# Kernel optimization log

Hardware: AMD Instinct MI355X
Metric: run time of the kernel (lower is better)

## Reference

```python
import jax, jax.numpy as jnp
import numpy as np

B, L, H, W = 16, 16, 64, 64
NUM_CODES = 64


def setup_inputs() -> dict:
    key = jax.random.key(0)
    k1, k2 = jax.random.split(key)
    z = jax.random.normal(k1, (B, L, H, W), dtype=jnp.float32)
    # nn.Embedding(latent_dim, num_codes).weight -> [latent_dim, num_codes]
    codes_w = jax.random.normal(k2, (L, NUM_CODES), dtype=jnp.float32)
    return {"z": z, "codes_w": codes_w}


def reference(z, codes_w):
    # z: [B, L, H, W] -> h: [B, H, W, L]
    h = jnp.transpose(z, (0, 2, 3, 1))
    # broadcast abs-distance to every code: [B, H, W, L, C]
    distances = jnp.abs(h[..., None] - codes_w)
    # Softmin over code axis == softmax of negated distances
    symbol_probs = jax.nn.softmax(-distances, axis=-1)
    # soft quantization: probability-weighted codebook values -> [B, H, W, L]
    soft_symbols = jnp.sum(symbol_probs * codes_w, axis=-1)
    # hard assignment: nearest code per (position, latent channel)
    idxes = jnp.argmin(distances, axis=-1)  # [B, H, W, L] int
    # gather codebook value per latent row (equivalent of take with row offsets)
    hard_symbols = jnp.take_along_axis(
        codes_w[None, None, None], idxes[..., None], axis=4
    )[..., 0]
    return soft_symbols, hard_symbols, idxes
```

## Files before the change

### kernel.cpp

```cpp
#include <hip/hip_runtime.h>


namespace {
constexpr int kL = 16;
constexpr int kC = 64;
constexpr int kHW = 64 * 64;
constexpr int kN = 16 * kHW * kL;
constexpr int kStride = 68;
constexpr float kLog2e = 1.44269504088896340736f;
}

__global__ __launch_bounds__(256) void soft_to_hard_kernel(
    const float* __restrict__ z,
    const float* __restrict__ codes,
    float* __restrict__ out)
{
    __shared__ float wl[kL * kStride];
    __shared__ float pl[kL * kStride];
    __shared__ float ql[kL * kStride];

    const int tid = threadIdx.x;

    {
        const int base = tid << 2;
        const int l = base >> 6;
        const int c = base & 63;
        const float4 wv = *reinterpret_cast<const float4*>(codes + base);
        const int o = l * kStride + c;
        wl[o + 0] = wv.x; wl[o + 1] = wv.y; wl[o + 2] = wv.z; wl[o + 3] = wv.w;
        pl[o + 0] = exp2f(wv.x * kLog2e);
        pl[o + 1] = exp2f(wv.y * kLog2e);
        pl[o + 2] = exp2f(wv.z * kLog2e);
        pl[o + 3] = exp2f(wv.w * kLog2e);
        ql[o + 0] = exp2f(-wv.x * kLog2e);
        ql[o + 1] = exp2f(-wv.y * kLog2e);
        ql[o + 2] = exp2f(-wv.z * kLog2e);
        ql[o + 3] = exp2f(-wv.w * kLog2e);
    }
    __syncthreads();

    const int gid = blockIdx.x * 256 + tid;
    const int l   = gid & (kL - 1);
    const int bhw = gid >> 4;
    const int b   = gid >> 16;
    const int hw  = bhw & (kHW - 1);

    const float zv = z[(b << 16) + (l << 12) + hw];

    const float t    = zv * kLog2e;
    const float E    = exp2f(t);
    const float Einv = exp2f(-t);

    const float* __restrict__ wr = wl + l * kStride;
    const float* __restrict__ pr = pl + l * kStride;
    const float* __restrict__ qr = ql + l * kStride;

    float mind = 3.4e38f;
    int   idx  = 0;
    float sum  = 0.0f;
    float wsum = 0.0f;

#define STEP(wc, pc, qc, cc)                                  \
    {                                                         \
        const float d = __builtin_fabsf(zv - (wc));           \
        idx  = (d < mind) ? (cc) : idx;                       \
        mind = fminf(d, mind);                                \
        const float e = fminf(E * (qc), Einv * (pc));         \
        sum += e;                                             \
        wsum = __builtin_fmaf(e, (wc), wsum);                 \
    }

#pragma unroll
    for (int c0 = 0; c0 < kC; c0 += 4) {
        const float4 wv = *reinterpret_cast<const float4*>(wr + c0);
        const float4 pv = *reinterpret_cast<const float4*>(pr + c0);
        const float4 qv = *reinterpret_cast<const float4*>(qr + c0);
        STEP(wv.x, pv.x, qv.x, c0 + 0);
        STEP(wv.y, pv.y, qv.y, c0 + 1);
        STEP(wv.z, pv.z, qv.z, c0 + 2);
        STEP(wv.w, pv.w, qv.w, c0 + 3);
    }
#undef STEP

    const float soft = wsum / sum;
    const float hard = wr[idx];

    out[gid]          = soft;
    out[kN + gid]     = hard;
    out[2 * kN + gid] = (float)idx;
}

extern "C" void kernel_launch(void* const* d_in, const int* in_sizes, int n_in,
                              void* d_out, int out_size, void* d_ws, size_t ws_size,
                              hipStream_t stream) {
    const float* z     = (const float*)d_in[0];
    const float* codes = (const float*)d_in[1];
    float* out = (float*)d_out;

    const int threads = 256;
    const int blocks  = kN / threads;
    soft_to_hard_kernel<<<blocks, threads, 0, stream>>>(z, codes, out);
}
```

Measured before the change: 72.11 us.

## Replace per-element code scan with sorted codebook, binary search and prefix-sum softmin

Each block sorts every codebook row in shared memory with a rank sort, resolves tie indices, and builds forward and backward prefix sums of exp(±w) and w·exp(±w). Each element then binary-searches its sorted row, computes the softmin sums from the two prefix tables with two exps, and picks the nearest code from the two neighbours. Each thread handles 8 elements across batches, with 512 blocks instead of 4096. This removes the 64-code inner loop per element, at the cost of per-block sort and table setup, and of prefix sums whose rounding differs from direct summation.

```diff
diff --git a/kernel.cpp b/kernel.cpp
--- a/kernel.cpp
+++ b/kernel.cpp
@@ -3,91 +3,150 @@
 
 namespace {
 constexpr int kL = 16;
-constexpr int kC = 64;
-constexpr int kHW = 64 * 64;
-constexpr int kN = 16 * kHW * kL;
-constexpr int kStride = 68;
+constexpr int kHW = 4096;
+constexpr int kN = 1 << 20;
+constexpr int kRow = 66;
+constexpr int kKRow = 65;
+constexpr int kTStride = kL * kRow + 12;
 constexpr float kLog2e = 1.44269504088896340736f;
 }
 
-__global__ __launch_bounds__(256) void soft_to_hard_kernel(
+__global__ __launch_bounds__(256) void soft_to_hard_fused(
     const float* __restrict__ z,
     const float* __restrict__ codes,
     float* __restrict__ out)
 {
-    __shared__ float wl[kL * kStride];
-    __shared__ float pl[kL * kStride];
-    __shared__ float ql[kL * kStride];
+    __shared__ unsigned long long K[kL * kKRow];
+    __shared__ float SW[kL * kRow];
+    __shared__ float RP[kL * kRow];
+    __shared__ float tabs[4 * kTStride];
 
     const int tid = threadIdx.x;
+    const int row = tid >> 4;
+    const int c0  = (tid & 15) << 2;
 
-    {
-        const int base = tid << 2;
-        const int l = base >> 6;
-        const int c = base & 63;
-        const float4 wv = *reinterpret_cast<const float4*>(codes + base);
-        const int o = l * kStride + c;
-        wl[o + 0] = wv.x; wl[o + 1] = wv.y; wl[o + 2] = wv.z; wl[o + 3] = wv.w;
-        pl[o + 0] = exp2f(wv.x * kLog2e);
-        pl[o + 1] = exp2f(wv.y * kLog2e);
-        pl[o + 2] = exp2f(wv.z * kLog2e);
-        pl[o + 3] = exp2f(wv.w * kLog2e);
-        ql[o + 0] = exp2f(-wv.x * kLog2e);
-        ql[o + 1] = exp2f(-wv.y * kLog2e);
-        ql[o + 2] = exp2f(-wv.z * kLog2e);
-        ql[o + 3] = exp2f(-wv.w * kLog2e);
+    const float4 wv = *reinterpret_cast<const float4*>(codes + (row << 6) + c0);
+    float v4[4] = {wv.x, wv.y, wv.z, wv.w};
+    unsigned long long myk[4];
+#pragma unroll
+    for (int k = 0; k < 4; ++k) {
+        unsigned int u = __float_as_uint(v4[k]);
+        u ^= (u & 0x80000000u) ? 0xFFFFFFFFu : 0x80000000u;
+        myk[k] = ((unsigned long long)u << 6) | (unsigned long long)(c0 + k);
+        K[row * kKRow + c0 + k] = myk[k];
+    }
+    if (tid < kL) {
+        SW[tid * kRow + 0]  = -3.0e38f;  RP[tid * kRow + 0]  = 1.0e9f;
+        SW[tid * kRow + 65] =  3.0e38f;  RP[tid * kRow + 65] = 1.0e9f;
     }
     __syncthreads();
 
-    const int gid = blockIdx.x * 256 + tid;
-    const int l   = gid & (kL - 1);
-    const int bhw = gid >> 4;
-    const int b   = gid >> 16;
-    const int hw  = bhw & (kHW - 1);
+    {
+        int r[4] = {0, 0, 0, 0};
+        const unsigned long long* Kr = K + row * kKRow;
+#pragma unroll 16
+        for (int c2 = 0; c2 < 64; ++c2) {
+            const unsigned long long k2 = Kr[c2];
+#pragma unroll
+            for (int k = 0; k < 4; ++k) r[k] += (k2 < myk[k]);
+        }
+#pragma unroll
+        for (int k = 0; k < 4; ++k) {
+            SW[row * kRow + r[k] + 1] = v4[k];
+            RP[row * kRow + r[k] + 1] = (float)(c0 + k);
+        }
+    }
+    __syncthreads();
 
-    const float zv = z[(b << 16) + (l << 12) + hw];
+    for (int pass = 0; pass < 2; ++pass) {
+        float nrep[4];
+#pragma unroll
+        for (int k = 0; k < 4; ++k) {
+            const int o = row * kRow + c0 + k + 1;
+            const float a = SW[o], b = SW[o - 1];
+            nrep[k] = (a == b) ? fminf(RP[o], RP[o - 1]) : RP[o];
+        }
+        __syncthreads();
+#pragma unroll
+        for (int k = 0; k < 4; ++k) RP[row * kRow + c0 + k + 1] = nrep[k];
+        __syncthreads();
+    }
 
-    const float t    = zv * kLog2e;
-    const float E    = exp2f(t);
-    const float Einv = exp2f(-t);
+    if (tid < 64) {
+        const int drow = tid >> 2;
+        const int kind = tid & 3;
+        const bool fwd = kind < 2;
+        const bool wgt = (kind & 1) != 0;
+        float* T = tabs + kind * kTStride + drow * kRow;
+        const float* S = SW + drow * kRow;
+        const float sgn = fwd ? kLog2e : -kLog2e;
+        float acc = 0.0f;
+        T[fwd ? 0 : 64] = 0.0f;
+        T[65] = 0.0f;
+#pragma unroll 8
+        for (int t = 1; t <= 64; ++t) {
+            const int i = fwd ? t : 65 - t;
+            const float v = S[i];
+            const float e = exp2f(v * sgn);
+            acc += wgt ? e * v : e;
+            T[fwd ? i : i - 1] = acc;
+        }
+    }
+    __syncthreads();
 
-    const float* __restrict__ wr = wl + l * kStride;
-    const float* __restrict__ pr = pl + l * kStride;
-    const float* __restrict__ qr = ql + l * kStride;
+    const int g0  = blockIdx.x * 256 + tid;
+    const int l   = g0 & 15;
+    const int hw  = (g0 >> 4) & (kHW - 1);
+    const int b0  = g0 >> 16;
+    const int lrow = l * kRow;
+    const float* SWr = SW + lrow;
+    const float* RPr = RP + lrow;
 
-    float mind = 3.4e38f;
-    int   idx  = 0;
-    float sum  = 0.0f;
-    float wsum = 0.0f;
+    float zv[8];
+#pragma unroll
+    for (int k = 0; k < 8; ++k)
+        zv[k] = z[((b0 + 2 * k) << 16) + (l << 12) + hw];
 
-#define STEP(wc, pc, qc, cc)                                  \
-    {                                                         \
-        const float d = __builtin_fabsf(zv - (wc));           \
-        idx  = (d < mind) ? (cc) : idx;                       \
-        mind = fminf(d, mind);                                \
-        const float e = fminf(E * (qc), Einv * (pc));         \
-        sum += e;                                             \
-        wsum = __builtin_fmaf(e, (wc), wsum);                 \
+    int p[8];
+#pragma unroll
+    for (int k = 0; k < 8; ++k) p[k] = 0;
+
+#pragma unroll
+    for (int step = 64; step >= 1; step >>= 1) {
+#pragma unroll
+        for (int k = 0; k < 8; ++k) {
+            const int t = p[k] + step;
+            const float v = SWr[(t <= 64) ? t : 64];
+            p[k] = (t <= 64 && v <= zv[k]) ? t : p[k];
+        }
     }
 
 #pragma unroll
-    for (int c0 = 0; c0 < kC; c0 += 4) {
-        const float4 wv = *reinterpret_cast<const float4*>(wr + c0);
-        const float4 pv = *reinterpret_cast<const float4*>(pr + c0);
-        const float4 qv = *reinterpret_cast<const float4*>(qr + c0);
-        STEP(wv.x, pv.x, qv.x, c0 + 0);
-        STEP(wv.y, pv.y, qv.y, c0 + 1);
-        STEP(wv.z, pv.z, qv.z, c0 + 2);
-        STEP(wv.w, pv.w, qv.w, c0 + 3);
+    for (int k = 0; k < 8; ++k) {
+        const int o = p[k];
+        const float vlo = SWr[o], vhi = SWr[o + 1];
+        const float rlo = RPr[o], rhi = RPr[o + 1];
+        const int to = lrow + o;
+        const float pp = tabs[to];
+        const float pw = tabs[kTStride + to];
+        const float qs = tabs[2 * kTStride + to];
+        const float qw = tabs[3 * kTStride + to];
+
+        const float t    = zv[k] * kLog2e;
+        const float E    = exp2f(t);
+        const float Einv = exp2f(-t);
+        const float sum  = __builtin_fmaf(Einv, pp, E * qs);
+        const float wsum = __builtin_fmaf(Einv, pw, E * qw);
+
+        const float dlo = __builtin_fabsf(zv[k] - vlo);
+        const float dhi = __builtin_fabsf(vhi - zv[k]);
+        const bool takelo = (dlo < dhi) || (dlo == dhi && rlo < rhi);
+
+        const int e = g0 + (k << 17);
+        out[e]           = wsum * __builtin_amdgcn_rcpf(sum);
+        out[kN + e]      = takelo ? vlo : vhi;
+        out[2 * kN + e]  = takelo ? rlo : rhi;
     }
-#undef STEP
-
-    const float soft = wsum / sum;
-    const float hard = wr[idx];
-
-    out[gid]          = soft;
-    out[kN + gid]     = hard;
-    out[2 * kN + gid] = (float)idx;
 }
 
 extern "C" void kernel_launch(void* const* d_in, const int* in_sizes, int n_in,
@@ -97,7 +156,5 @@
     const float* codes = (const float*)d_in[1];
     float* out = (float*)d_out;
 
-    const int threads = 256;
-    const int blocks  = kN / threads;
-    soft_to_hard_kernel<<<blocks, threads, 0, stream>>>(z, codes, out);
+    soft_to_hard_fused<<<512, 256, 0, stream>>>(z, codes, out);
 }
```

Result: no change. 72.29 us (+0.3%).
